# Kernel optimization log

Hardware: AMD Instinct MI355X
Metric: run time of the kernel (lower is better)

## Reference

```python
import jax, jax.numpy as jnp
import numpy as np

HEADS, DIM_HEAD, LANDMARKS, PINV_ITERS, CONV_K = 8, 64, 256, 6, 33


def iter_pinv(x, iters=PINV_ITERS):
    # Moore-Penrose iterative pseudo-inverse (lucidrains nystrom_attention)
    abs_x = jnp.abs(x)
    scale = abs_x.sum(-1).max() * abs_x.sum(-2).max()  # global maxes, as in torch.max
    z = jnp.swapaxes(x, -1, -2) / scale
    I = jnp.eye(x.shape[-1], dtype=x.dtype)
    for _ in range(iters):
        xz = x @ z
        z = 0.25 * z @ (13.0 * I - xz @ (15.0 * I - xz @ (7.0 * I - xz)))
    return z


def nystrom_attention(h, W_qkv, W_out, b_out, conv_w):
    b, n, _ = h.shape
    inner = HEADS * DIM_HEAD
    qkv = h @ W_qkv  # (b, n, 3*inner), bias=False
    q, k, v = jnp.split(qkv, 3, axis=-1)
    split_heads = lambda t: t.reshape(b, n, HEADS, DIM_HEAD).transpose(0, 2, 1, 3)
    q, k, v = split_heads(q), split_heads(k), split_heads(v)  # (b,h,n,dh)
    q = q * (DIM_HEAD ** -0.5)
    l = n // LANDMARKS  # tokens per landmark (n divisible by m, so no padding)
    q_l = q.reshape(b, HEADS, LANDMARKS, l, DIM_HEAD).mean(3)
    k_l = k.reshape(b, HEADS, LANDMARKS, l, DIM_HEAD).mean(3)
    sim1 = jnp.einsum('bhnd,bhmd->bhnm', q, k_l)      # (b,h,n,m)
    sim2 = jnp.einsum('bhmd,bhld->bhml', q_l, k_l)    # (b,h,m,m)
    sim3 = jnp.einsum('bhmd,bhnd->bhmn', q_l, k)      # (b,h,m,n)
    attn1 = jax.nn.softmax(sim1, -1)
    attn2 = jax.nn.softmax(sim2, -1)
    attn3 = jax.nn.softmax(sim3, -1)
    out = (attn1 @ iter_pinv(attn2)) @ (attn3 @ v)    # (b,h,n,dh)
    # residual depthwise conv along sequence dim: Conv2d(heads, heads, (33,1), groups=heads, no bias)
    res = jax.lax.conv_general_dilated(
        v, conv_w, window_strides=(1, 1),
        padding=((CONV_K // 2, CONV_K // 2), (0, 0)),
        feature_group_count=HEADS)
    out = out + res
    out = out.transpose(0, 2, 1, 3).reshape(b, n, inner)
    return out @ W_out + b_out


def setup_inputs() -> dict:
    key = jax.random.key(0)
    ks = jax.random.split(key, 8)
    N, Din, Dout = 8192, 1024, 256
    inner = HEADS * DIM_HEAD
    s = 0.02
    return {
        'x': jax.random.normal(ks[0], (1, N, Din), jnp.float32),
        'W_ft': jax.random.normal(ks[1], (Din, Dout), jnp.float32) * s,
        'b_ft': jnp.zeros((Dout,), jnp.float32),
        'W_qkv': jax.random.normal(ks[2], (Dout, 3 * inner), jnp.float32) * s,
        'W_out': jax.random.normal(ks[3], (inner, Dout), jnp.float32) * s,
        'b_out': jnp.zeros((Dout,), jnp.float32),
        'conv_w': jax.random.normal(ks[4], (HEADS, 1, CONV_K, 1), jnp.float32) * s,
        'W_score': jax.random.normal(ks[5], (Dout, 1), jnp.float32) * s,
        'b_score': jnp.zeros((1,), jnp.float32),
    }


def reference(x, W_ft, b_ft, W_qkv, W_out, b_out, conv_w, W_score, b_score):
    # feature_transform: Linear -> Dropout (identity in eval) -> ReLU
    h = jax.nn.relu(x @ W_ft + b_ft)                 # (1, N, Dout)
    af = nystrom_attention(h, W_qkv, W_out, b_out, conv_w)
    # score_layer: Linear -> Dropout -> ReLU
    scores = jax.nn.relu(af @ W_score + b_score)     # (1, N, 1)
    scores = scores[0].T                             # (1, N)
    weights = jax.nn.softmax(scores, axis=1)         # (1, N)
    aggregated = weights @ h[0]                      # (1, Dout)
    return aggregated, weights
```

## Files before the change

kernel.cpp:

```cpp
#include <hip/hip_runtime.h>

typedef unsigned short u16;
typedef __attribute__((ext_vector_type(8))) short s16x8;
typedef __attribute__((ext_vector_type(4))) float f32x4;
typedef __attribute__((ext_vector_type(8))) unsigned short u16x8;

__device__ inline float b2f(u16 u) {
  unsigned x = ((unsigned)u) << 16;
  return __builtin_bit_cast(float, x);
}
__device__ inline u16 f2b(float f) {
  unsigned u = __builtin_bit_cast(unsigned, f);
  u += 0x7fffu + ((u >> 16) & 1u);
  return (u16)(u >> 16);
}

#define GLL(src, dst) __builtin_amdgcn_global_load_lds( \
    (const __attribute__((address_space(1))) unsigned int*)(src), \
    (__attribute__((address_space(3))) unsigned int*)(dst), 16, 0, 0)

struct MP {
  const u16* A; const u16* B;
  u16* C; u16* Ct; float* Cf; u16* vTo;
  const u16* Aadd; const float* bias;
// ... 167 lines not shown
  const int bz = blockIdx.z, head = bz >> 4, kc = bz & 15;
  const u16* S = p.S + (size_t)head * 256 * 8192 + kc * 512;
  const u16* B = p.vT + (size_t)head * 524288 + kc * 512;
  const int m0 = blockIdx.y * 128;
  const int srow = lane & 15, skoff = (lane >> 4) * 8;
  const int wm0 = (wid >> 1) * 64, wn0 = (wid & 1) * 32;

  int rowA[2]; float am[2], ai[2];
#pragma unroll
  for (int ap = 0; ap < 2; ap++) {
    rowA[ap] = m0 + (wid + ap * 4) * 16 + srow;
    float2 s2 = p.st[head * 256 + rowA[ap]];
    am[ap] = s2.x; ai[ap] = s2.y;
  }

  f32x4 acc[4][2];
#pragma unroll
  for (int i = 0; i < 4; i++)
#pragma unroll
    for (int j = 0; j < 2; j++) acc[i][j] = (f32x4){0.f, 0.f, 0.f, 0.f};

  u16x8 areg[2];
  auto load_a = [&](int kt) {
#pragma unroll
    for (int ap = 0; ap < 2; ap++)
      areg[ap] = *(const u16x8*)(S + (size_t)rowA[ap] * 8192 + kt + skoff);
  };
  auto write_a = [&](int sb) {
#pragma unroll
    for (int ap = 0; ap < 2; ap++) {
      int pp = wid + ap * 4;
      u16 t[8];
#pragma unroll
      for (int e = 0; e < 8; e++)
        t[e] = f2b(expf(b2f(areg[ap][e]) - am[ap]) * ai[ap]);
      *(s16x8*)&lds[sb * (NPAN * 512) + pp * 512 + lane * 8] = *(const s16x8*)t;
    }
  };
  auto stage_b = [&](int sb, int kt) {
    int pp = 8 + wid;
    const u16* src = B + (size_t)((pp - 8) * 16 + srow) * 8192 + kt + skoff;
    GLL(src, &lds[sb * (NPAN * 512) + pp * 512]);
  };
  auto compute = [&](int sb) {
    const int bo = sb * (NPAN * 512);
    s16x8 afr[4], bfr[2];
#pragma unroll
    for (int i = 0; i < 4; i++)
      afr[i] = *(const s16x8*)&lds[bo + (wm0 / 16 + i) * 512 + lane * 8];
#pragma unroll
    for (int j = 0; j < 2; j++)
      bfr[j] = *(const s16x8*)&lds[bo + (APAN + wn0 / 16 + j) * 512 + lane * 8];
#pragma unroll
    for (int i = 0; i < 4; i++)
#pragma unroll
      for (int j = 0; j < 2; j++)
        acc[i][j] = __builtin_amdgcn_mfma_f32_16x16x32_bf16(afr[i], bfr[j], acc[i][j], 0, 0, 0);
  };

  const int nt = 16;
  int buf = 0;
  load_a(0); stage_b(0, 0); write_a(0);
  asm volatile("s_waitcnt vmcnt(0)" ::: "memory");
  __syncthreads();
  for (int t = 0; t < nt; ++t) {
    if (t + 1 < nt) { load_a((t + 1) * 32); stage_b(buf ^ 1, (t + 1) * 32); }
    compute(buf);
    if (t + 1 < nt) write_a(buf ^ 1);
    asm volatile("s_waitcnt vmcnt(0)" ::: "memory");
    __syncthreads();
    buf ^= 1;
  }

  const int r0 = (lane >> 4) * 4, c0 = lane & 15;
#pragma unroll
  for (int i = 0; i < 4; i++)
#pragma unroll
    for (int j = 0; j < 2; j++)
#pragma unroll
      for (int q = 0; q < 4; q++) {
        const int gr = m0 + wm0 + i * 16 + r0 + q;
        const int gc = wn0 + j * 16 + c0;
        p.Cf[(size_t)bz * 16384 + (size_t)gr * 64 + gc] = acc[i][j][q];
      }
}

struct FA1 { const u16 *qkvb, *kl, *MmT; u16 *af; };

__global__ __launch_bounds__(256) void fused_attn1(FA1 p)
{
  __shared__ __align__(16) u16 lds[36864];
  __shared__ float mb[4][64];
  const int tid = threadIdx.x, lane = tid & 63, wid = tid >> 6;
  const int head = blockIdx.y, n0 = blockIdx.x * 64;
  const int srow = lane & 15, skoff = (lane >> 4) * 8;
  const int rbase = (lane >> 4) * 4;

  for (int pid = wid; pid < 72; pid += 4) {
    const u16* src;
    if (pid < 8) {
      int pr = pid >> 1, kc = pid & 1;
      src = p.qkvb + (size_t)(n0 + pr * 16 + srow) * 1536 + head * 64 + kc * 32 + skoff;
    } else if (pid < 40) {
      int j = pid - 8, pr = j >> 1, kc = j & 1;
      src = p.kl + head * 16384 + (size_t)(pr * 16 + srow) * 64 + kc * 32 + skoff;
    } else {
      int j = pid - 40, pr = j >> 3, kc = j & 7;
      src = p.MmT + head * 16384 + (size_t)(pr * 16 + srow) * 256 + kc * 32 + skoff;
    }
    GLL(src, &lds[pid * 512]);
  }
  asm volatile("s_waitcnt vmcnt(0)" ::: "memory");
  __syncthreads();

  const int wr = (wid >> 1) * 32, ch_ = wid & 1;
  f32x4 s[2][8];
#pragma unroll
  for (int i = 0; i < 2; i++)
#pragma unroll
    for (int j = 0; j < 8; j++) s[i][j] = (f32x4){0.f, 0.f, 0.f, 0.f};
#pragma unroll
  for (int t = 0; t < 2; t++) {
    s16x8 a[2], b[8];
#pragma unroll
    for (int i = 0; i < 2; i++)
      a[i] = *(const s16x8*)&lds[(((wid >> 1) * 2 + i) * 2 + t) * 512 + lane * 8];
#pragma unroll
    for (int j = 0; j < 8; j++)
      b[j] = *(const s16x8*)&lds[4096 + ((ch_ * 8 + j) * 2 + t) * 512 + lane * 8];
#pragma unroll
    for (int i = 0; i < 2; i++)
#pragma unroll
      for (int j = 0; j < 8; j++)
        s[i][j] = __builtin_amdgcn_mfma_f32_16x16x32_bf16(a[i], b[j], s[i][j], 0, 0, 0);
  }
#pragma unroll
  for (int i = 0; i < 2; i++)
#pragma unroll
    for (int q = 0; q < 4; q++) {
      float rm = -INFINITY;
#pragma unroll
      for (int j = 0; j < 8; j++) rm = fmaxf(rm, s[i][j][q]);
#pragma unroll
      for (int off = 1; off < 16; off <<= 1) rm = fmaxf(rm, __shfl_xor(rm, off));
      if ((lane & 15) == 0) mb[ch_][wr + i * 16 + rbase + q] = rm;
    }
  __syncthreads();
  float m_[2][4];
#pragma unroll
  for (int i = 0; i < 2; i++)
#pragma unroll
    for (int q = 0; q < 4; q++)
      m_[i][q] = fmaxf(mb[0][wr + i * 16 + rbase + q], mb[1][wr + i * 16 + rbase + q]);
#pragma unroll
  for (int i = 0; i < 2; i++)
#pragma unroll
    for (int q = 0; q < 4; q++) {
      float ss = 0.f;
#pragma unroll
      for (int j = 0; j < 8; j++) {
        float e = expf(s[i][j][q] - m_[i][q]);
        s[i][j][q] = e; ss += e;
      }
#pragma unroll
      for (int off = 1; off < 16; off <<= 1) ss += __shfl_xor(ss, off);
      if ((lane & 15) == 0) mb[2 + ch_][wr + i * 16 + rbase + q] = ss;
    }
  __syncthreads();
#pragma unroll
  for (int i = 0; i < 2; i++)
#pragma unroll
    for (int q = 0; q < 4; q++) {
      int row = wr + i * 16 + rbase + q;
      float inv = 1.f / (mb[2][row] + mb[3][row]);
#pragma unroll
      for (int j = 0; j < 8; j++)
        lds[(size_t)row * 264 + ch_ * 128 + j * 16 + (lane & 15)] = f2b(s[i][j][q] * inv);
    }
  __syncthreads();
  const int wr2 = (wid >> 1) * 32, wd2 = (wid & 1) * 32;
  f32x4 acc[2][2];
#pragma unroll
  for (int i = 0; i < 2; i++)
#pragma unroll
    for (int jd = 0; jd < 2; jd++) acc[i][jd] = (f32x4){0.f, 0.f, 0.f, 0.f};
#pragma unroll
  for (int t = 0; t < 8; t++) {
    s16x8 a[2], b[2];
#pragma unroll
    for (int i = 0; i < 2; i++)
      a[i] = *(const s16x8*)&lds[(size_t)(wr2 + i * 16 + (lane & 15)) * 264 + t * 32 + (lane >> 4) * 8];
#pragma unroll
    for (int jd = 0; jd < 2; jd++)
      b[jd] = *(const s16x8*)&lds[20480 + (((wid & 1) * 2 + jd) * 8 + t) * 512 + lane * 8];
#pragma unroll
    for (int i = 0; i < 2; i++)
#pragma unroll
      for (int jd = 0; jd < 2; jd++)
        acc[i][jd] = __builtin_amdgcn_mfma_f32_16x16x32_bf16(a[i], b[jd], acc[i][jd], 0, 0, 0);
  }
#pragma unroll
  for (int i = 0; i < 2; i++)
#pragma unroll
    for (int jd = 0; jd < 2; jd++)
#pragma unroll
      for (int q = 0; q < 4; q++)
        p.af[(size_t)(n0 + wr2 + i * 16 + rbase + q) * 512 + head * 64 + wd2 + jd * 16 + (lane & 15)]
            = f2b(acc[i][jd][q]);
}

__global__ void conv_res_add_bf16(const u16* __restrict__ qkvb,
                                  const float* __restrict__ convw,
                                  u16* __restrict__ af)
{
  __shared__ float vt[96][64];
  const int h = blockIdx.y, n0 = blockIdx.x * 64;
  const int t = threadIdx.x, ch = t & 63, r0 = t >> 6;
  for (int r = r0; r < 96; r += 4) {
    int n = n0 - 16 + r;
    float v = 0.f;
    if (n >= 0 && n < 8192) v = b2f(qkvb[(size_t)n * 1536 + 1024 + h * 64 + ch]);
    vt[r][ch] = v;
  }
  __syncthreads();
  float w[33];
#pragma unroll
  for (int j = 0; j < 33; j++) w[j] = convw[h * 33 + j];
  for (int tl = r0; tl < 64; tl += 4) {
    float acc = 0.f;
#pragma unroll
    for (int j = 0; j < 33; j++) acc += w[j] * vt[tl + j][ch];
    size_t o = (size_t)(n0 + tl) * 512 + h * 64 + ch;
    af[o] = f2b(b2f(af[o]) + acc);
  }
}

__global__ void reduce_bias_bf16(const float* __restrict__ parts, int nparts,
                                 const float* __restrict__ bias, int relu,
                                 u16* __restrict__ out,
                                 const float* __restrict__ Wscore,
                                 const float* __restrict__ bscore,
                                 float* __restrict__ scores)
{
  const int i4 = blockIdx.x * 256 + threadIdx.x;
  float4 s = ((const float4*)parts)[i4];
  for (int k = 1; k < nparts; k++) {
    float4 v = ((const float4*)parts)[(size_t)k * 524288 + i4];
    s.x += v.x; s.y += v.y; s.z += v.z; s.w += v.w;
  }
  const float4 b = ((const float4*)bias)[i4 & 63];
  s.x += b.x; s.y += b.y; s.z += b.z; s.w += b.w;
  if (relu) {
    s.x = fmaxf(s.x, 0.f); s.y = fmaxf(s.y, 0.f);
    s.z = fmaxf(s.z, 0.f); s.w = fmaxf(s.w, 0.f);
  }
  if (out) {
    ushort4 o; o.x = f2b(s.x); o.y = f2b(s.y); o.z = f2b(s.z); o.w = f2b(s.w);
    ((ushort4*)out)[i4] = o;
  }
  if (Wscore) {
    const int lane = threadIdx.x & 63;
    const float4 w = ((const float4*)Wscore)[lane];
    float v = s.x * w.x + s.y * w.y + s.z * w.z + s.w * w.w;
    for (int off = 32; off; off >>= 1) v += __shfl_down(v, off);
    if (lane == 0)
      scores[blockIdx.x * 4 + (threadIdx.x >> 6)] = fmaxf(v + bscore[0], 0.f);
  }
}

__global__ void fused_tail(const float* __restrict__ scores,
                           const u16* __restrict__ hb, float* __restrict__ out)
{
  __shared__ float red[256];
  const int t = threadIdx.x, c = blockIdx.x;
  float e[32];
  float m = -INFINITY;
#pragma unroll
  for (int i = 0; i < 32; i++) { e[i] = scores[t + i * 256]; m = fmaxf(m, e[i]); }
  red[t] = m; __syncthreads();
  for (int s = 128; s; s >>= 1) { if (t < s) red[t] = fmaxf(red[t], red[t + s]); __syncthreads(); }
  m = red[0]; __syncthreads();
  float ls = 0.f;
#pragma unroll
  for (int i = 0; i < 32; i++) { e[i] = expf(e[i] - m); ls += e[i]; }
  red[t] = ls; __syncthreads();
  for (int s = 128; s; s >>= 1) { if (t < s) red[t] += red[t + s]; __syncthreads(); }
  const float inv = 1.f / red[0];
  __syncthreads();

  if (c < 256) {
    float acc = 0.f;
#pragma unroll
    for (int i = 0; i < 32; i++)
      acc += e[i] * inv * b2f(hb[(size_t)(t + i * 256) * 256 + c]);
    red[t] = acc; __syncthreads();
    for (int s = 128; s; s >>= 1) { if (t < s) red[t] += red[t + s]; __syncthreads(); }
    if (t == 0) out[c] = red[0];
  } else {
#pragma unroll
    for (int i = 0; i < 32; i++) out[256 + t + i * 256] = e[i] * inv;
  }
}

__global__ void prescale(const u16* __restrict__ x2, float* __restrict__ sbuf)
{
  const int h = blockIdx.x, t = threadIdx.x;
  const u16* X = x2 + ((size_t)h << 16);
  float cs = 0.f;
  for (int r = 0; r < 256; r++) cs += fabsf(b2f(X[r * 256 + t]));
  float rs = 0.f;
  for (int c4 = 0; c4 < 256; c4 += 4) {
    ushort4 v = *(const ushort4*)(X + (size_t)t * 256 + c4);
    rs += fabsf(b2f(v.x)) + fabsf(b2f(v.y)) + fabsf(b2f(v.z)) + fabsf(b2f(v.w));
  }
  __shared__ float red[512];
  red[t] = rs; red[256 + t] = cs;
  __syncthreads();
  for (int s = 128; s; s >>= 1) {
    if (t < s) {
      red[t] = fmaxf(red[t], red[t + s]);
      red[256 + t] = fmaxf(red[256 + t], red[256 + t + s]);
    }
    __syncthreads();
  }
  if (t == 0) { sbuf[h] = red[0]; sbuf[8 + h] = red[256]; }
}

__global__ void pinv_init(const u16* __restrict__ x2, const float* __restrict__ sbuf,
                          u16* __restrict__ z0, u16* __restrict__ z0T)
{
  __shared__ u16 tile[64][80];
  const int t = threadIdx.x;
  const size_t base = (size_t)blockIdx.y << 16;
  const int tr = (blockIdx.x >> 2) * 64, tc = (blockIdx.x & 3) * 64;
  const u16* X = x2 + base;

  float mr = -INFINITY, mc = -INFINITY;
#pragma unroll
  for (int i = 0; i < 8; i++) {
    mr = fmaxf(mr, sbuf[i]);
    mc = fmaxf(mc, sbuf[8 + i]);
  }
  const float inv = 1.f / (mr * mc);

  {
    int r = t >> 2, cg = (t & 3) * 16;
#pragma unroll
    for (int v4 = 0; v4 < 4; v4++) {
      ushort4 v = *(const ushort4*)(X + (size_t)(tr + r) * 256 + tc + cg + v4 * 4);
      v.x = f2b(b2f(v.x) * inv); v.y = f2b(b2f(v.y) * inv);
      v.z = f2b(b2f(v.z) * inv); v.w = f2b(b2f(v.w) * inv);
      *(ushort4*)(z0T + base + (size_t)(tr + r) * 256 + tc + cg + v4 * 4) = v;
      *(ushort4*)&tile[r][cg + v4 * 4] = v;
    }
  }
  __syncthreads();
  {
    int c = t >> 2, rg = (t & 3) * 16;
    u16 o[16];
#pragma unroll
    for (int e = 0; e < 16; e++) o[e] = tile[rg + e][c];
#pragma unroll
    for (int v4 = 0; v4 < 4; v4++)
      *(ushort4*)(z0 + base + (size_t)(tc + c) * 256 + tr + rg + v4 * 4) = *(ushort4*)&o[v4 * 4];
  }
}

struct PG {
  const u16 *U, *V, *Xadd, *XaddT;
  u16 *DR, *DT;
  float alpha, beta;
};

template<bool WD, bool WDT>
__global__ __launch_bounds__(256) void pinv_gemm(PG p)
{
  __shared__ __align__(16) u16 lds[65536 / 2];
  const int tid = threadIdx.x, lane = tid & 63, wid = tid >> 6;
  const size_t base = (size_t)blockIdx.z << 16;
  const u16* U = p.U + base;
  const u16* V = p.V + base;
  const int m0 = blockIdx.y * 64, n0 = blockIdx.x * 64;
  const int srow = lane & 15, skoff = (lane >> 4) * 8;
  const int wr = (wid >> 1) * 32, wc = (wid & 1) * 32;

#pragma unroll
  for (int q = 0; q < 16; q++) {
    const int pid = wid * 16 + q;
    const int rg = (pid >> 3) & 3, t = pid & 7;
    const u16* src = (pid < 32)
      ? U + (size_t)(m0 + rg * 16 + srow) * 256 + t * 32 + skoff
      : V + (size_t)(n0 + rg * 16 + srow) * 256 + t * 32 + skoff;
    GLL(src, &lds[pid * 512]);
  }
  asm volatile("s_waitcnt vmcnt(0)" ::: "memory");
  __syncthreads();

  f32x4 acc[2][2], accT[2][2];
#pragma unroll
  for (int i = 0; i < 2; i++)
#pragma unroll
    for (int j = 0; j < 2; j++) {
      acc[i][j] = (f32x4){0.f, 0.f, 0.f, 0.f};
      accT[i][j] = (f32x4){0.f, 0.f, 0.f, 0.f};
    }

#pragma unroll
  for (int t = 0; t < 8; t++) {
    s16x8 afr[2], bfr[2];
#pragma unroll
    for (int i = 0; i < 2; i++)
      afr[i] = *(const s16x8*)&lds[((wr / 16 + i) * 8 + t) * 512 + lane * 8];
#pragma unroll
    for (int j = 0; j < 2; j++)
      bfr[j] = *(const s16x8*)&lds[(32 + (wc / 16 + j) * 8 + t) * 512 + lane * 8];
#pragma unroll
    for (int i = 0; i < 2; i++)
#pragma unroll
      for (int j = 0; j < 2; j++) {
        if constexpr (WD)
          acc[i][j] = __builtin_amdgcn_mfma_f32_16x16x32_bf16(afr[i], bfr[j], acc[i][j], 0, 0, 0);
        if constexpr (WDT)
          accT[j][i] = __builtin_amdgcn_mfma_f32_16x16x32_bf16(bfr[j], afr[i], accT[j][i], 0, 0, 0);
      }
  }

  const int r0 = (lane >> 4) * 4, c0 = lane & 15;
  if constexpr (WD) {
    const u16* Xa = p.Xadd ? p.Xadd + base : nullptr;
    u16* DR = p.DR + base;
#pragma unroll
    for (int i = 0; i < 2; i++)
#pragma unroll
      for (int j = 0; j < 2; j++)
#pragma unroll
        for (int q = 0; q < 4; q++) {
          const int gr = m0 + wr + i * 16 + r0 + q;
          const int gc = n0 + wc + j * 16 + c0;
          float v = p.alpha * acc[i][j][q];
          if (Xa) v += p.beta * b2f(Xa[(size_t)gr * 256 + gc]);
          DR[(size_t)gr * 256 + gc] = f2b(v);
        }
  }
  if constexpr (WDT) {
    const u16* Xt = p.XaddT ? p.XaddT + base : nullptr;
    u16* DT = p.DT + base;
#pragma unroll
    for (int j = 0; j < 2; j++)
#pragma unroll
      for (int i = 0; i < 2; i++)
#pragma unroll
        for (int q = 0; q < 4; q++) {
          const int gn = n0 + wc + j * 16 + r0 + q;
          const int gm = m0 + wr + i * 16 + c0;
          float v = p.alpha * accT[j][i][q];
          if (Xt) v += p.beta * b2f(Xt[(size_t)gn * 256 + gm]);
          DT[(size_t)gn * 256 + gm] = f2b(v);
        }
  }
}

struct PR1 { const u16 *A, *At, *z; u16 *B, *Bt, *G, *Gt, *W; };

__global__ __launch_bounds__(256) void pinv_r1(PR1 p)
{
  __shared__ __align__(16) u16 lds[32768];
  const int tid = threadIdx.x, lane = tid & 63, wid = tid >> 6;
  const int prob = blockIdx.z >> 3;
  const size_t base = (size_t)(blockIdx.z & 7) << 16;
  const u16* U = (prob ? p.z : p.A) + base;
  const u16* V = p.At + base;
  const int m0 = blockIdx.y * 64, n0 = blockIdx.x * 64;
  const int srow = lane & 15, skoff = (lane >> 4) * 8;
  const int wr = (wid >> 1) * 32, wc = (wid & 1) * 32;

#pragma unroll
  for (int q = 0; q < 16; q++) {
    const int pid = wid * 16 + q;
    const int rg = (pid >> 3) & 3, t = pid & 7;
    const u16* src = (pid < 32)
      ? U + (size_t)(m0 + rg * 16 + srow) * 256 + t * 32 + skoff
      : V + (size_t)(n0 + rg * 16 + srow) * 256 + t * 32 + skoff;
    GLL(src, &lds[pid * 512]);
  }
  asm volatile("s_waitcnt vmcnt(0)" ::: "memory");
  __syncthreads();

  f32x4 acc[2][2], accT[2][2];
#pragma unroll
  for (int i = 0; i < 2; i++)
#pragma unroll
    for (int j = 0; j < 2; j++) {
      acc[i][j] = (f32x4){0.f, 0.f, 0.f, 0.f};
      accT[i][j] = (f32x4){0.f, 0.f, 0.f, 0.f};
    }

#pragma unroll
  for (int t = 0; t < 8; t++) {
    s16x8 afr[2], bfr[2];
#pragma unroll
    for (int i = 0; i < 2; i++)
      afr[i] = *(const s16x8*)&lds[((wr / 16 + i) * 8 + t) * 512 + lane * 8];
#pragma unroll
    for (int j = 0; j < 2; j++)
      bfr[j] = *(const s16x8*)&lds[(32 + (wc / 16 + j) * 8 + t) * 512 + lane * 8];
#pragma unroll
    for (int i = 0; i < 2; i++)
#pragma unroll
      for (int j = 0; j < 2; j++) {
        acc[i][j] = __builtin_amdgcn_mfma_f32_16x16x32_bf16(afr[i], bfr[j], acc[i][j], 0, 0, 0);
        if (prob == 0)
          accT[j][i] = __builtin_amdgcn_mfma_f32_16x16x32_bf16(bfr[j], afr[i], accT[j][i], 0, 0, 0);
      }
  }

  const int r0 = (lane >> 4) * 4, c0 = lane & 15;
  if (prob == 0) {
    const u16* Ab  = p.A  + base;
    const u16* Atb = p.At + base;
    u16 *Bv = p.B + base, *Btv = p.Bt + base;
    u16 *Gv = p.G + base, *Gtv = p.Gt + base;
#pragma unroll
    for (int i = 0; i < 2; i++)
#pragma unroll
      for (int j = 0; j < 2; j++)
#pragma unroll
        for (int q = 0; q < 4; q++) {
          const int gr = m0 + wr + i * 16 + r0 + q;
          const int gc = n0 + wc + j * 16 + c0;
          float b = acc[i][j][q];
          float a = b2f(Ab[(size_t)gr * 256 + gc]);
          Bv[(size_t)gr * 256 + gc] = f2b(b);
          Gv[(size_t)gr * 256 + gc] = f2b(7.f * a - b);
        }
#pragma unroll
    for (int j = 0; j < 2; j++)
#pragma unroll
      for (int i = 0; i < 2; i++)
#pragma unroll
        for (int q = 0; q < 4; q++) {
          const int gn = n0 + wc + j * 16 + r0 + q;
          const int gm = m0 + wr + i * 16 + c0;
          float bt = accT[j][i][q];
          float at = b2f(Atb[(size_t)gn * 256 + gm]);
          Btv[(size_t)gn * 256 + gm] = f2b(bt);
          Gtv[(size_t)gn * 256 + gm] = f2b(7.f * at - bt);
        }
  } else {
    u16* Wv = p.W + base;
#pragma unroll
    for (int i = 0; i < 2; i++)
#pragma unroll
      for (int j = 0; j < 2; j++)
#pragma unroll
        for (int q = 0; q < 4; q++) {
          const int gr = m0 + wr + i * 16 + r0 + q;
          const int gc = n0 + wc + j * 16 + c0;
          Wv[(size_t)gr * 256 + gc] = f2b(acc[i][j][q]);
        }
  }
}

struct PR2 { const u16 *W, *G, *Gt, *B, *Bt, *z, *A, *At; u16 *zo, *Ao, *Aot; };

__global__ __launch_bounds__(256) void pinv_r2(PR2 p)
{
  __shared__ __align__(16) u16 lds[32768];
  const int tid = threadIdx.x, lane = tid & 63, wid = tid >> 6;
  const int prob = blockIdx.z >> 3;
  const size_t base = (size_t)(blockIdx.z & 7) << 16;
  const u16* U = (prob ? p.G  : p.W ) + base;
  const u16* V = (prob ? p.Bt : p.Gt) + base;
  const int m0 = blockIdx.y * 64, n0 = blockIdx.x * 64;
  const int srow = lane & 15, skoff = (lane >> 4) * 8;
  const int wr = (wid >> 1) * 32, wc = (wid & 1) * 32;

#pragma unroll
  for (int q = 0; q < 16; q++) {
    const int pid = wid * 16 + q;
    const int rg = (pid >> 3) & 3, t = pid & 7;
    const u16* src = (pid < 32)
      ? U + (size_t)(m0 + rg * 16 + srow) * 256 + t * 32 + skoff
      : V + (size_t)(n0 + rg * 16 + srow) * 256 + t * 32 + skoff;
    GLL(src, &lds[pid * 512]);
  }
  asm volatile("s_waitcnt vmcnt(0)" ::: "memory");
  __syncthreads();

  f32x4 acc[2][2], accT[2][2];
#pragma unroll
  for (int i = 0; i < 2; i++)
#pragma unroll
    for (int j = 0; j < 2; j++) {
      acc[i][j] = (f32x4){0.f, 0.f, 0.f, 0.f};
      accT[i][j] = (f32x4){0.f, 0.f, 0.f, 0.f};
    }

#pragma unroll
  for (int t = 0; t < 8; t++) {
    s16x8 afr[2], bfr[2];
#pragma unroll
    for (int i = 0; i < 2; i++)
      afr[i] = *(const s16x8*)&lds[((wr / 16 + i) * 8 + t) * 512 + lane * 8];
#pragma unroll
    for (int j = 0; j < 2; j++)
      bfr[j] = *(const s16x8*)&lds[(32 + (wc / 16 + j) * 8 + t) * 512 + lane * 8];
#pragma unroll
    for (int i = 0; i < 2; i++)
#pragma unroll
      for (int j = 0; j < 2; j++) {
        acc[i][j] = __builtin_amdgcn_mfma_f32_16x16x32_bf16(afr[i], bfr[j], acc[i][j], 0, 0, 0);
        if (prob)
          accT[j][i] = __builtin_amdgcn_mfma_f32_16x16x32_bf16(bfr[j], afr[i], accT[j][i], 0, 0, 0);
      }
  }

  const int r0 = (lane >> 4) * 4, c0 = lane & 15;
  if (prob == 0) {
    const u16* Zb = p.z + base;
    const u16* Wb = p.W + base;
    u16* Zo = p.zo + base;
#pragma unroll
    for (int i = 0; i < 2; i++)
#pragma unroll
      for (int j = 0; j < 2; j++)
#pragma unroll
        for (int q = 0; q < 4; q++) {
          const int gr = m0 + wr + i * 16 + r0 + q;
          const int gc = n0 + wc + j * 16 + c0;
          float v = 0.25f * acc[i][j][q]
                  + 3.25f * b2f(Zb[(size_t)gr * 256 + gc])
                  - 3.75f * b2f(Wb[(size_t)gr * 256 + gc]);
          Zo[(size_t)gr * 256 + gc] = f2b(v);
        }
  } else {
    const u16* Ab  = p.A  + base;
    const u16* Bb  = p.B  + base;
    const u16* Atb = p.At + base;
    const u16* Btb = p.Bt + base;
    u16* Ao  = p.Ao  + base;
    u16* Aot = p.Aot + base;
#pragma unroll
    for (int i = 0; i < 2; i++)
#pragma unroll
      for (int j = 0; j < 2; j++)
#pragma unroll
        for (int q = 0; q < 4; q++) {
          const int gr = m0 + wr + i * 16 + r0 + q;
          const int gc = n0 + wc + j * 16 + c0;
          float v = 0.25f * acc[i][j][q]
                  + 3.25f * b2f(Ab[(size_t)gr * 256 + gc])
                  - 3.75f * b2f(Bb[(size_t)gr * 256 + gc]);
          Ao[(size_t)gr * 256 + gc] = f2b(v);
        }
#pragma unroll
    for (int j = 0; j < 2; j++)
#pragma unroll
      for (int i = 0; i < 2; i++)
#pragma unroll
        for (int q = 0; q < 4; q++) {
          const int gn = n0 + wc + j * 16 + r0 + q;
          const int gm = m0 + wr + i * 16 + c0;
          float v = 0.25f * accT[j][i][q]
                  + 3.25f * b2f(Atb[(size_t)gn * 256 + gm])
                  - 3.75f * b2f(Btb[(size_t)gn * 256 + gm]);
          Aot[(size_t)gn * 256 + gm] = f2b(v);
        }
  }
}

__global__ void prep_weights(const float* __restrict__ Wft, const float* __restrict__ Wqkv,
                             const float* __restrict__ Wout, u16* __restrict__ WftT,
                             u16* __restrict__ WqkvT, u16* __restrict__ WoutT)
{
  int idx = blockIdx.x * 256 + threadIdx.x;
  if (idx < 262144) {
    int r = idx & 1023, c = idx >> 10;
    WftT[idx] = f2b(Wft[(size_t)r * 256 + c]);
  } else if (idx < 655360) {
    int i = idx - 262144;
    int r = i & 255, c = i >> 8;
    WqkvT[i] = f2b(Wqkv[(size_t)r * 1536 + c]);
  } else {
    int i = idx - 655360;
    int r = i & 511, c = i >> 9;
    WoutT[i] = f2b(Wout[(size_t)r * 256 + c]);
  }
}

__global__ void landmark_means(const u16* __restrict__ qkvb,
                               u16* __restrict__ ql, u16* __restrict__ kl)
{
  int idx = blockIdx.x * 256 + threadIdx.x;
  int which = idx >> 17, r = idx & 131071;
  int h = r >> 14, m = (r >> 6) & 255, d = r & 63;
  const u16* src = qkvb + (which ? 512 : 0) + h * 64 + d;
  float s = 0.f; int n0 = m * 32;
  for (int i = 0; i < 32; i++) s += b2f(src[(size_t)(n0 + i) * 1536]);
  (which ? kl : ql)[r] = f2b(s * (1.f / 32.f));
}

__global__ void softmax_rows_bf16_256(u16* __restrict__ d)
{
  const int row = blockIdx.x * 4 + (threadIdx.x >> 6);
  const int lane = threadIdx.x & 63;
  ushort4* p = (ushort4*)(d + (size_t)row * 256);
  ushort4 raw = p[lane];
  float v0 = b2f(raw.x), v1 = b2f(raw.y), v2 = b2f(raw.z), v3 = b2f(raw.w);
  float mx = fmaxf(fmaxf(v0, v1), fmaxf(v2, v3));
  for (int off = 1; off < 64; off <<= 1) mx = fmaxf(mx, __shfl_xor(mx, off));
  v0 = expf(v0 - mx); v1 = expf(v1 - mx); v2 = expf(v2 - mx); v3 = expf(v3 - mx);
  float s = v0 + v1 + v2 + v3;
  for (int off = 1; off < 64; off <<= 1) s += __shfl_xor(s, off);
  float inv = 1.f / s;
  raw.x = f2b(v0 * inv); raw.y = f2b(v1 * inv); raw.z = f2b(v2 * inv); raw.w = f2b(v3 * inv);
  p[lane] = raw;
}

__global__ void reduce_avT(const float* __restrict__ avp, u16* __restrict__ avT)
{
  int idx = blockIdx.x * 256 + threadIdx.x;
  int m = idx & 255, d = (idx >> 8) & 63, h = idx >> 14;
  float s = 0.f;
  for (int c = 0; c < 16; c++) s += avp[((size_t)(h * 16 + c)) * 16384 + m * 64 + d];
  avT[((size_t)h * 64 + d) * 256 + m] = f2b(s);
}

extern "C" void kernel_launch(void* const* d_in, const int* in_sizes, int n_in,
                              void* d_out, int out_size, void* d_ws, size_t ws_size,
                              hipStream_t stream)
{
  const float* x       = (const float*)d_in[0];
  const float* W_ft    = (const float*)d_in[1];
  const float* b_ft    = (const float*)d_in[2];
  const float* W_qkv   = (const float*)d_in[3];
  const float* W_out   = (const float*)d_in[4];
  const float* b_out   = (const float*)d_in[5];
  const float* conv_w  = (const float*)d_in[6];
  const float* W_score = (const float*)d_in[7];
  const float* b_score = (const float*)d_in[8];
  float* out = (float*)d_out;

  char* W = (char*)d_ws;
  auto alloc = [&](size_t bytes) { char* r = W; W += (bytes + 255) & ~(size_t)255; return r; };
  u16* WftT  = (u16*)alloc(256ull * 1024 * 2);
  u16* WqkvT = (u16*)alloc(1536ull * 256 * 2);
  u16* WoutT = (u16*)alloc(256ull * 512 * 2);
  u16* hb    = (u16*)alloc(8192ull * 256 * 2);
  u16* qkvb  = (u16*)alloc(8192ull * 1536 * 2);
  u16* ql    = (u16*)alloc(8ull * 256 * 64 * 2);
  u16* kl    = (u16*)alloc(8ull * 256 * 64 * 2);
  u16* x2    = (u16*)alloc(8ull * 256 * 256 * 2);
  u16* z0    = (u16*)alloc(8ull * 256 * 256 * 2);
  u16* z0T   = (u16*)alloc(8ull * 256 * 256 * 2);
  u16* zp    = (u16*)alloc(8ull * 256 * 256 * 2);
  u16* Amat  = (u16*)alloc(8ull * 256 * 256 * 2);
  u16* AmatT = (u16*)alloc(8ull * 256 * 256 * 2);
  u16* Am2   = (u16*)alloc(8ull * 256 * 256 * 2);
  u16* Am2T  = (u16*)alloc(8ull * 256 * 256 * 2);
  u16* Bm    = (u16*)alloc(8ull * 256 * 256 * 2);
  u16* BmT   = (u16*)alloc(8ull * 256 * 256 * 2);
  u16* Gm    = (u16*)alloc(8ull * 256 * 256 * 2);
  u16* GmT   = (u16*)alloc(8ull * 256 * 256 * 2);
  u16* Wm    = (u16*)alloc(8ull * 256 * 256 * 2);
  u16* BUF   = (u16*)alloc(8ull * 8192 * 256 * 2);
  u16* vT    = (u16*)alloc(8ull * 64 * 8192 * 2);
  float* avp = (float*)alloc(8ull * 16 * 256 * 64 * 4);
  u16* avT   = (u16*)alloc(8ull * 64 * 256 * 2);
  u16* MmT   = (u16*)alloc(8ull * 64 * 256 * 2);
  u16* af    = (u16*)alloc(8192ull * 512 * 2);
  float* gpart = (float*)alloc(4ull * 8192 * 256 * 4);
  float2* stat = (float2*)alloc(2048 * 8);
  float* sbuf   = (float*)alloc(256);
  float* scores = (float*)alloc(8192 * 4);

  auto mp = [](const u16* A, const u16* B, int M, int N, int K,
               int lda, int ldb, long long bA, long long bB) {
    MP p{}; p.A = A; p.B = B; p.M = M; p.N = N; p.K = K;
    p.lda = lda; p.ldb = ldb; p.bA = bA; p.bB = bB;
    p.alpha = 1.f; p.beta = 0.f; p.kchunks = 1; return p;
  };

  prep_weights<<<3072, 256, 0, stream>>>(W_ft, W_qkv, W_out, WftT, WqkvT, WoutT);

  { MP p = mp((const u16*)x, WftT, 8192, 256, 256, 1024, 1024, 0, 0);
    p.kchunks = 4; p.Cf = gpart; p.ldcf = 256; p.bCf = 2097152;
    gemm_mfma<64, 256, true><<<dim3(1, 128, 4), 256, 0, stream>>>(p); }
  reduce_bias_bf16<<<2048, 256, 0, stream>>>(gpart, 4, b_ft, 1, hb,
                                             nullptr, nullptr, nullptr);

  { MP p = mp(hb, WqkvT, 8192, 1536, 256, 256, 256, 0, 0);
    p.C = qkvb; p.ldc = 1536; p.scale_cols = 512; p.colscale = 0.125f; p.vTo = vT;
    gemm_mfma<128, 128, false><<<dim3(12, 64, 1), 256, 0, stream>>>(p); }

  landmark_means<<<1024, 256, 0, stream>>>(qkvb, ql, kl);

  { MP p = mp(ql, kl, 256, 256, 64, 64, 64, 16384, 16384);
    p.C = x2; p.ldc = 256; p.bC = 65536;
    gemm_mfma<64, 64, false><<<dim3(4, 4, 8), 256, 0, stream>>>(p); }
  softmax_rows_bf16_256<<<512, 256, 0, stream>>>(x2);

  prescale<<<8, 256, 0, stream>>>(x2, sbuf);
  pinv_init<<<dim3(16, 8), 256, 0, stream>>>(x2, sbuf, z0, z0T);
  { PG p{x2, z0T, nullptr, nullptr, Amat, AmatT, 1.f, 0.f};
    pinv_gemm<true, true><<<dim3(4, 4, 8), 256, 0, stream>>>(p); }
  {
    const dim3 b(256);
    u16 *zr = z0, *zo = zp;
    u16 *Ar = Amat, *Art = AmatT, *Ao = Am2, *Aot = Am2T;
    for (int it = 0; it < 6; it++) {
      { PR1 r{Ar, Art, zr, Bm, BmT, Gm, GmT, Wm};
        pinv_r1<<<dim3(4, 4, 16), b, 0, stream>>>(r); }
      { PR2 r{Wm, Gm, GmT, Bm, BmT, zr, Ar, Art, zo, Ao, Aot};
        pinv_r2<<<dim3(4, 4, (it == 5) ? 8 : 16), b, 0, stream>>>(r); }
      u16* t;
      t = zr; zr = zo; zo = t;
      t = Ar; Ar = Ao; Ao = t;
      t = Art; Art = Aot; Aot = t;
    }
  }

  { MP p = mp(ql, qkvb + 512, 256, 8192, 64, 64, 1536, 16384, 64);
    p.C = BUF; p.ldc = 8192; p.bC = (long long)256 * 8192;
    gemm_mfma<128, 128, false><<<dim3(64, 2, 8), 256, 0, stream>>>(p); }
  row_stats_8192<<<2048, 256, 0, stream>>>(BUF, stat);

  { AVP p{BUF, stat, vT, avp};
    av_gemm_exp<<<dim3(1, 2, 128), 256, 0, stream>>>(p); }
  reduce_avT<<<512, 256, 0, stream>>>(avp, avT);

  { MP p = mp(z0, avT, 256, 64, 256, 256, 256, 65536, 16384);
    p.Ct = MmT; p.ldct = 256; p.bCt = 16384;
    gemm_mfma<64, 64, false><<<dim3(1, 4, 8), 256, 0, stream>>>(p); }

  { FA1 fp{qkvb, kl, MmT, af};
    fused_attn1<<<dim3(128, 8), 256, 0, stream>>>(fp); }

  conv_res_add_bf16<<<dim3(128, 8), 256, 0, stream>>>(qkvb, conv_w, af);

  { MP p = mp(af, WoutT, 8192, 256, 128, 512, 512, 0, 0);
    p.kchunks = 4; p.Cf = gpart; p.ldcf = 256; p.bCf = 2097152;
    gemm_mfma<64, 256, false><<<dim3(1, 128, 4), 256, 0, stream>>>(p); }
  reduce_bias_bf16<<<2048, 256, 0, stream>>>(gpart, 4, b_out, 0, nullptr,
                                             W_score, b_score, scores);

  fused_tail<<<257, 256, 0, stream>>>(scores, hb, out);
}
```

Measured before the change: 379.1 us.

## Fuse pinv prescale, init and iterations into one persistent kernel with grid barriers

Replaces the 15 separate launches for the iterative pseudo-inverse (prescale, init, first gemm, and six pairs of r1/r2 gemms) with a single persistent kernel of 256 blocks. Stages are separated by a software grid barrier built on an atomic counter, which prep_weights resets to zero at the start. This is meant to remove per-launch overhead and the tail gaps between small dependent kernels. The trade-off is that correctness depends on all 256 blocks being resident at once, and every stage now pays an atomic-spin barrier across the whole grid.

```diff
diff --git a/kernel.cpp b/kernel.cpp
--- a/kernel.cpp
+++ b/kernel.cpp
@@ -493,9 +493,30 @@
   }
 }
 
-__global__ void prescale(const u16* __restrict__ x2, float* __restrict__ sbuf)
-{
-  const int h = blockIdx.x, t = threadIdx.x;
+struct PP {
+  const u16* x2; float* sbuf;
+  u16 *z0, *z0T, *zp;
+  u16 *Am, *AmT, *Am2, *Am2T;
+  u16 *B, *Bt, *G, *Gt, *W;
+  unsigned* cnt;
+};
+
+__device__ __forceinline__ void gbar(unsigned* cnt, unsigned target)
+{
+  __syncthreads();
+  if (threadIdx.x == 0) {
+    __threadfence();
+    __hip_atomic_fetch_add(cnt, 1u, __ATOMIC_RELAXED, __HIP_MEMORY_SCOPE_AGENT);
+    while (__hip_atomic_load(cnt, __ATOMIC_RELAXED, __HIP_MEMORY_SCOPE_AGENT) < target)
+      __builtin_amdgcn_s_sleep(2);
+    __threadfence();
+  }
+  __syncthreads();
+}
+
+__device__ __forceinline__ void prescale_body(const u16* x2, float* sbuf,
+                                              int h, int t, float* red)
+{
   const u16* X = x2 + ((size_t)h << 16);
   float cs = 0.f;
   for (int r = 0; r < 256; r++) cs += fabsf(b2f(X[r * 256 + t]));
@@ -504,7 +525,6 @@
     ushort4 v = *(const ushort4*)(X + (size_t)t * 256 + c4);
     rs += fabsf(b2f(v.x)) + fabsf(b2f(v.y)) + fabsf(b2f(v.z)) + fabsf(b2f(v.w));
   }
-  __shared__ float red[512];
   red[t] = rs; red[256 + t] = cs;
   __syncthreads();
   for (int s = 128; s; s >>= 1) {
@@ -517,13 +537,13 @@
   if (t == 0) { sbuf[h] = red[0]; sbuf[8 + h] = red[256]; }
 }
 
-__global__ void pinv_init(const u16* __restrict__ x2, const float* __restrict__ sbuf,
-                          u16* __restrict__ z0, u16* __restrict__ z0T)
-{
-  __shared__ u16 tile[64][80];
-  const int t = threadIdx.x;
-  const size_t base = (size_t)blockIdx.y << 16;
-  const int tr = (blockIdx.x >> 2) * 64, tc = (blockIdx.x & 3) * 64;
+__device__ __forceinline__ void init_body(const u16* x2, const float* sbuf,
+                                          u16* z0, u16* z0T, int tileIdx, int head,
+                                          int t, u16* smem)
+{
+  u16 (*tile)[80] = reinterpret_cast<u16(*)[80]>(smem);
+  const size_t base = (size_t)head << 16;
+  const int tr = (tileIdx >> 2) * 64, tc = (tileIdx & 3) * 64;
   const u16* X = x2 + base;
 
   float mr = -INFINITY, mc = -INFINITY;
@@ -557,37 +577,24 @@
   }
 }
 
-struct PG {
-  const u16 *U, *V, *Xadd, *XaddT;
-  u16 *DR, *DT;
-  float alpha, beta;
-};
-
-template<bool WD, bool WDT>
-__global__ __launch_bounds__(256) void pinv_gemm(PG p)
-{
-  __shared__ __align__(16) u16 lds[65536 / 2];
-  const int tid = threadIdx.x, lane = tid & 63, wid = tid >> 6;
-  const size_t base = (size_t)blockIdx.z << 16;
-  const u16* U = p.U + base;
-  const u16* V = p.V + base;
-  const int m0 = blockIdx.y * 64, n0 = blockIdx.x * 64;
+__device__ __forceinline__ void pgemm(const u16* U, const u16* V, u16* lds,
+                                      int m0, int n0, int lane, int wid, bool doT,
+                                      f32x4 (&acc)[2][2], f32x4 (&accT)[2][2])
+{
   const int srow = lane & 15, skoff = (lane >> 4) * 8;
-  const int wr = (wid >> 1) * 32, wc = (wid & 1) * 32;
-
 #pragma unroll
   for (int q = 0; q < 16; q++) {
     const int pid = wid * 16 + q;
-    const int rg = (pid >> 3) & 3, t = pid & 7;
+    const int rg = (pid >> 3) & 3, tt = pid & 7;
     const u16* src = (pid < 32)
-      ? U + (size_t)(m0 + rg * 16 + srow) * 256 + t * 32 + skoff
-      : V + (size_t)(n0 + rg * 16 + srow) * 256 + t * 32 + skoff;
+      ? U + (size_t)(m0 + rg * 16 + srow) * 256 + tt * 32 + skoff
+      : V + (size_t)(n0 + rg * 16 + srow) * 256 + tt * 32 + skoff;
     GLL(src, &lds[pid * 512]);
   }
   asm volatile("s_waitcnt vmcnt(0)" ::: "memory");
   __syncthreads();
 
-  f32x4 acc[2][2], accT[2][2];
+  const int wr = (wid >> 1) * 32, wc = (wid & 1) * 32;
 #pragma unroll
   for (int i = 0; i < 2; i++)
 #pragma unroll
@@ -595,7 +602,6 @@
       acc[i][j] = (f32x4){0.f, 0.f, 0.f, 0.f};
       accT[i][j] = (f32x4){0.f, 0.f, 0.f, 0.f};
     }
-
 #pragma unroll
   for (int t = 0; t < 8; t++) {
     s16x8 afr[2], bfr[2];
@@ -609,17 +615,37 @@
     for (int i = 0; i < 2; i++)
 #pragma unroll
       for (int j = 0; j < 2; j++) {
-        if constexpr (WD)
-          acc[i][j] = __builtin_amdgcn_mfma_f32_16x16x32_bf16(afr[i], bfr[j], acc[i][j], 0, 0, 0);
-        if constexpr (WDT)
+        acc[i][j] = __builtin_amdgcn_mfma_f32_16x16x32_bf16(afr[i], bfr[j], acc[i][j], 0, 0, 0);
+        if (doT)
           accT[j][i] = __builtin_amdgcn_mfma_f32_16x16x32_bf16(bfr[j], afr[i], accT[j][i], 0, 0, 0);
       }
   }
-
+}
+
+__global__ __launch_bounds__(256) void pinv_persist(PP p)
+{
+  __shared__ __align__(16) u16 smem[16384];
+  const int bid = blockIdx.x, tid = threadIdx.x;
+  const int lane = tid & 63, wid = tid >> 6;
+  unsigned* cnt = p.cnt;
+
+  if (bid < 8) prescale_body(p.x2, p.sbuf, bid, tid, (float*)smem);
+  gbar(cnt, 256u);
+
+  if (bid < 128) init_body(p.x2, p.sbuf, p.z0, p.z0T, bid & 15, bid >> 4, tid, smem);
+  gbar(cnt, 512u);
+
+  const int bx = bid & 3, by = (bid >> 2) & 3, bz = bid >> 4;
+  const int m0 = by * 64, n0 = bx * 64;
+  const int wr = (wid >> 1) * 32, wc = (wid & 1) * 32;
   const int r0 = (lane >> 4) * 4, c0 = lane & 15;
-  if constexpr (WD) {
-    const u16* Xa = p.Xadd ? p.Xadd + base : nullptr;
-    u16* DR = p.DR + base;
+
+  if (bid < 128) {
+    const size_t base = (size_t)bz << 16;
+    f32x4 acc[2][2], accT[2][2];
+    pgemm(p.x2 + base, p.z0T + base, smem, m0, n0, lane, wid, true, acc, accT);
+    u16* DR = p.Am + base;
+    u16* DT = p.AmT + base;
 #pragma unroll
     for (int i = 0; i < 2; i++)
 #pragma unroll
@@ -628,14 +654,8 @@
         for (int q = 0; q < 4; q++) {
           const int gr = m0 + wr + i * 16 + r0 + q;
           const int gc = n0 + wc + j * 16 + c0;
-          float v = p.alpha * acc[i][j][q];
-          if (Xa) v += p.beta * b2f(Xa[(size_t)gr * 256 + gc]);
-          DR[(size_t)gr * 256 + gc] = f2b(v);
+          DR[(size_t)gr * 256 + gc] = f2b(acc[i][j][q]);
         }
-  }
-  if constexpr (WDT) {
-    const u16* Xt = p.XaddT ? p.XaddT + base : nullptr;
-    u16* DT = p.DT + base;
 #pragma unroll
     for (int j = 0; j < 2; j++)
 #pragma unroll
@@ -644,227 +664,141 @@
         for (int q = 0; q < 4; q++) {
           const int gn = n0 + wc + j * 16 + r0 + q;
           const int gm = m0 + wr + i * 16 + c0;
-          float v = p.alpha * accT[j][i][q];
-          if (Xt) v += p.beta * b2f(Xt[(size_t)gn * 256 + gm]);
-          DT[(size_t)gn * 256 + gm] = f2b(v);
+          DT[(size_t)gn * 256 + gm] = f2b(accT[j][i][q]);
         }
   }
-}
-
-struct PR1 { const u16 *A, *At, *z; u16 *B, *Bt, *G, *Gt, *W; };
-
-__global__ __launch_bounds__(256) void pinv_r1(PR1 p)
-{
-  __shared__ __align__(16) u16 lds[32768];
-  const int tid = threadIdx.x, lane = tid & 63, wid = tid >> 6;
-  const int prob = blockIdx.z >> 3;
-  const size_t base = (size_t)(blockIdx.z & 7) << 16;
-  const u16* U = (prob ? p.z : p.A) + base;
-  const u16* V = p.At + base;
-  const int m0 = blockIdx.y * 64, n0 = blockIdx.x * 64;
-  const int srow = lane & 15, skoff = (lane >> 4) * 8;
-  const int wr = (wid >> 1) * 32, wc = (wid & 1) * 32;
-
-#pragma unroll
-  for (int q = 0; q < 16; q++) {
-    const int pid = wid * 16 + q;
-    const int rg = (pid >> 3) & 3, t = pid & 7;
-    const u16* src = (pid < 32)
-      ? U + (size_t)(m0 + rg * 16 + srow) * 256 + t * 32 + skoff
-      : V + (size_t)(n0 + rg * 16 + srow) * 256 + t * 32 + skoff;
-    GLL(src, &lds[pid * 512]);
-  }
-  asm volatile("s_waitcnt vmcnt(0)" ::: "memory");
-  __syncthreads();
-
-  f32x4 acc[2][2], accT[2][2];
-#pragma unroll
-  for (int i = 0; i < 2; i++)
-#pragma unroll
-    for (int j = 0; j < 2; j++) {
-      acc[i][j] = (f32x4){0.f, 0.f, 0.f, 0.f};
-      accT[i][j] = (f32x4){0.f, 0.f, 0.f, 0.f};
-    }
-
-#pragma unroll
-  for (int t = 0; t < 8; t++) {
-    s16x8 afr[2], bfr[2];
-#pragma unroll
-    for (int i = 0; i < 2; i++)
-      afr[i] = *(const s16x8*)&lds[((wr / 16 + i) * 8 + t) * 512 + lane * 8];
-#pragma unroll
-    for (int j = 0; j < 2; j++)
-      bfr[j] = *(const s16x8*)&lds[(32 + (wc / 16 + j) * 8 + t) * 512 + lane * 8];
-#pragma unroll
-    for (int i = 0; i < 2; i++)
-#pragma unroll
-      for (int j = 0; j < 2; j++) {
-        acc[i][j] = __builtin_amdgcn_mfma_f32_16x16x32_bf16(afr[i], bfr[j], acc[i][j], 0, 0, 0);
-        if (prob == 0)
-          accT[j][i] = __builtin_amdgcn_mfma_f32_16x16x32_bf16(bfr[j], afr[i], accT[j][i], 0, 0, 0);
+  unsigned tgt = 768u;
+  gbar(cnt, tgt);
+
+  u16 *zr = p.z0, *zo = p.zp;
+  u16 *Ar = p.Am, *Art = p.AmT, *Ao = p.Am2, *Aot = p.Am2T;
+  const int prob = bz >> 3;
+  const size_t base = (size_t)(bz & 7) << 16;
+
+  for (int it = 0; it < 6; it++) {
+    {
+      f32x4 acc[2][2], accT[2][2];
+      pgemm((prob ? zr : Ar) + base, Art + base, smem, m0, n0, lane, wid,
+            prob == 0, acc, accT);
+      if (prob == 0) {
+        const u16* Ab  = Ar  + base;
+        const u16* Atb = Art + base;
+        u16 *Bv = p.B + base, *Btv = p.Bt + base;
+        u16 *Gv = p.G + base, *Gtv = p.Gt + base;
+#pragma unroll
+        for (int i = 0; i < 2; i++)
+#pragma unroll
+          for (int j = 0; j < 2; j++)
+#pragma unroll
+            for (int q = 0; q < 4; q++) {
+              const int gr = m0 + wr + i * 16 + r0 + q;
+              const int gc = n0 + wc + j * 16 + c0;
+              float b = acc[i][j][q];
+              float a = b2f(Ab[(size_t)gr * 256 + gc]);
+              Bv[(size_t)gr * 256 + gc] = f2b(b);
+              Gv[(size_t)gr * 256 + gc] = f2b(7.f * a - b);
+            }
+#pragma unroll
+        for (int j = 0; j < 2; j++)
+#pragma unroll
+          for (int i = 0; i < 2; i++)
+#pragma unroll
+            for (int q = 0; q < 4; q++) {
+              const int gn = n0 + wc + j * 16 + r0 + q;
+              const int gm = m0 + wr + i * 16 + c0;
+              float bt = accT[j][i][q];
+              float at = b2f(Atb[(size_t)gn * 256 + gm]);
+              Btv[(size_t)gn * 256 + gm] = f2b(bt);
+              Gtv[(size_t)gn * 256 + gm] = f2b(7.f * at - bt);
+            }
+      } else {
+        u16* Wv = p.W + base;
+#pragma unroll
+        for (int i = 0; i < 2; i++)
+#pragma unroll
+          for (int j = 0; j < 2; j++)
+#pragma unroll
+            for (int q = 0; q < 4; q++) {
+              const int gr = m0 + wr + i * 16 + r0 + q;
+              const int gc = n0 + wc + j * 16 + c0;
+              Wv[(size_t)gr * 256 + gc] = f2b(acc[i][j][q]);
+            }
       }
-  }
-
-  const int r0 = (lane >> 4) * 4, c0 = lane & 15;
-  if (prob == 0) {
-    const u16* Ab  = p.A  + base;
-    const u16* Atb = p.At + base;
-    u16 *Bv = p.B + base, *Btv = p.Bt + base;
-    u16 *Gv = p.G + base, *Gtv = p.Gt + base;
-#pragma unroll
-    for (int i = 0; i < 2; i++)
-#pragma unroll
-      for (int j = 0; j < 2; j++)
-#pragma unroll
-        for (int q = 0; q < 4; q++) {
-          const int gr = m0 + wr + i * 16 + r0 + q;
-          const int gc = n0 + wc + j * 16 + c0;
-          float b = acc[i][j][q];
-          float a = b2f(Ab[(size_t)gr * 256 + gc]);
-          Bv[(size_t)gr * 256 + gc] = f2b(b);
-          Gv[(size_t)gr * 256 + gc] = f2b(7.f * a - b);
-        }
-#pragma unroll
-    for (int j = 0; j < 2; j++)
-#pragma unroll
-      for (int i = 0; i < 2; i++)
-#pragma unroll
-        for (int q = 0; q < 4; q++) {
-          const int gn = n0 + wc + j * 16 + r0 + q;
-          const int gm = m0 + wr + i * 16 + c0;
-          float bt = accT[j][i][q];
-          float at = b2f(Atb[(size_t)gn * 256 + gm]);
-          Btv[(size_t)gn * 256 + gm] = f2b(bt);
-          Gtv[(size_t)gn * 256 + gm] = f2b(7.f * at - bt);
-        }
-  } else {
-    u16* Wv = p.W + base;
-#pragma unroll
-    for (int i = 0; i < 2; i++)
-#pragma unroll
-      for (int j = 0; j < 2; j++)
-#pragma unroll
-        for (int q = 0; q < 4; q++) {
-          const int gr = m0 + wr + i * 16 + r0 + q;
-          const int gc = n0 + wc + j * 16 + c0;
-          Wv[(size_t)gr * 256 + gc] = f2b(acc[i][j][q]);
-        }
-  }
-}
-
-struct PR2 { const u16 *W, *G, *Gt, *B, *Bt, *z, *A, *At; u16 *zo, *Ao, *Aot; };
-
-__global__ __launch_bounds__(256) void pinv_r2(PR2 p)
-{
-  __shared__ __align__(16) u16 lds[32768];
-  const int tid = threadIdx.x, lane = tid & 63, wid = tid >> 6;
-  const int prob = blockIdx.z >> 3;
-  const size_t base = (size_t)(blockIdx.z & 7) << 16;
-  const u16* U = (prob ? p.G  : p.W ) + base;
-  const u16* V = (prob ? p.Bt : p.Gt) + base;
-  const int m0 = blockIdx.y * 64, n0 = blockIdx.x * 64;
-  const int srow = lane & 15, skoff = (lane >> 4) * 8;
-  const int wr = (wid >> 1) * 32, wc = (wid & 1) * 32;
-
-#pragma unroll
-  for (int q = 0; q < 16; q++) {
-    const int pid = wid * 16 + q;
-    const int rg = (pid >> 3) & 3, t = pid & 7;
-    const u16* src = (pid < 32)
-      ? U + (size_t)(m0 + rg * 16 + srow) * 256 + t * 32 + skoff
-      : V + (size_t)(n0 + rg * 16 + srow) * 256 + t * 32 + skoff;
-    GLL(src, &lds[pid * 512]);
-  }
-  asm volatile("s_waitcnt vmcnt(0)" ::: "memory");
-  __syncthreads();
-
-  f32x4 acc[2][2], accT[2][2];
-#pragma unroll
-  for (int i = 0; i < 2; i++)
-#pragma unroll
-    for (int j = 0; j < 2; j++) {
-      acc[i][j] = (f32x4){0.f, 0.f, 0.f, 0.f};
-      accT[i][j] = (f32x4){0.f, 0.f, 0.f, 0.f};
-    }
-
-#pragma unroll
-  for (int t = 0; t < 8; t++) {
-    s16x8 afr[2], bfr[2];
-#pragma unroll
-    for (int i = 0; i < 2; i++)
-      afr[i] = *(const s16x8*)&lds[((wr / 16 + i) * 8 + t) * 512 + lane * 8];
-#pragma unroll
-    for (int j = 0; j < 2; j++)
-      bfr[j] = *(const s16x8*)&lds[(32 + (wc / 16 + j) * 8 + t) * 512 + lane * 8];
-#pragma unroll
-    for (int i = 0; i < 2; i++)
-#pragma unroll
-      for (int j = 0; j < 2; j++) {
-        acc[i][j] = __builtin_amdgcn_mfma_f32_16x16x32_bf16(afr[i], bfr[j], acc[i][j], 0, 0, 0);
-        if (prob)
-          accT[j][i] = __builtin_amdgcn_mfma_f32_16x16x32_bf16(bfr[j], afr[i], accT[j][i], 0, 0, 0);
+    }
+    tgt += 256u; gbar(cnt, tgt);
+
+    if (!(it == 5 && prob == 1)) {
+      f32x4 acc[2][2], accT[2][2];
+      pgemm((prob ? p.G : p.W) + base, (prob ? p.Bt : p.Gt) + base, smem,
+            m0, n0, lane, wid, prob == 1, acc, accT);
+      if (prob == 0) {
+        const u16* Zb = zr + base;
+        const u16* Wb = p.W + base;
+        u16* Zo = zo + base;
+#pragma unroll
+        for (int i = 0; i < 2; i++)
+#pragma unroll
+          for (int j = 0; j < 2; j++)
+#pragma unroll
+            for (int q = 0; q < 4; q++) {
+              const int gr = m0 + wr + i * 16 + r0 + q;
+              const int gc = n0 + wc + j * 16 + c0;
+              float v = 0.25f * acc[i][j][q]
+                      + 3.25f * b2f(Zb[(size_t)gr * 256 + gc])
+                      - 3.75f * b2f(Wb[(size_t)gr * 256 + gc]);
+              Zo[(size_t)gr * 256 + gc] = f2b(v);
+            }
+      } else {
+        const u16* Ab  = Ar  + base;
+        const u16* Bb  = p.B + base;
+        const u16* Atb = Art + base;
+        const u16* Btb = p.Bt + base;
+        u16* AoP  = Ao  + base;
+        u16* AotP = Aot + base;
+#pragma unroll
+        for (int i = 0; i < 2; i++)
+#pragma unroll
+          for (int j = 0; j < 2; j++)
+#pragma unroll
+            for (int q = 0; q < 4; q++) {
+              const int gr = m0 + wr + i * 16 + r0 + q;
+              const int gc = n0 + wc + j * 16 + c0;
+              float v = 0.25f * acc[i][j][q]
+                      + 3.25f * b2f(Ab[(size_t)gr * 256 + gc])
+                      - 3.75f * b2f(Bb[(size_t)gr * 256 + gc]);
+              AoP[(size_t)gr * 256 + gc] = f2b(v);
+            }
+#pragma unroll
+        for (int j = 0; j < 2; j++)
+#pragma unroll
+          for (int i = 0; i < 2; i++)
+#pragma unroll
+            for (int q = 0; q < 4; q++) {
+              const int gn = n0 + wc + j * 16 + r0 + q;
+              const int gm = m0 + wr + i * 16 + c0;
+              float v = 0.25f * accT[j][i][q]
+                      + 3.25f * b2f(Atb[(size_t)gn * 256 + gm])
+                      - 3.75f * b2f(Btb[(size_t)gn * 256 + gm]);
+              AotP[(size_t)gn * 256 + gm] = f2b(v);
+            }
       }
-  }
-
-  const int r0 = (lane >> 4) * 4, c0 = lane & 15;
-  if (prob == 0) {
-    const u16* Zb = p.z + base;
-    const u16* Wb = p.W + base;
-    u16* Zo = p.zo + base;
-#pragma unroll
-    for (int i = 0; i < 2; i++)
-#pragma unroll
-      for (int j = 0; j < 2; j++)
-#pragma unroll
-        for (int q = 0; q < 4; q++) {
-          const int gr = m0 + wr + i * 16 + r0 + q;
-          const int gc = n0 + wc + j * 16 + c0;
-          float v = 0.25f * acc[i][j][q]
-                  + 3.25f * b2f(Zb[(size_t)gr * 256 + gc])
-                  - 3.75f * b2f(Wb[(size_t)gr * 256 + gc]);
-          Zo[(size_t)gr * 256 + gc] = f2b(v);
-        }
-  } else {
-    const u16* Ab  = p.A  + base;
-    const u16* Bb  = p.B  + base;
-    const u16* Atb = p.At + base;
-    const u16* Btb = p.Bt + base;
-    u16* Ao  = p.Ao  + base;
-    u16* Aot = p.Aot + base;
-#pragma unroll
-    for (int i = 0; i < 2; i++)
-#pragma unroll
-      for (int j = 0; j < 2; j++)
-#pragma unroll
-        for (int q = 0; q < 4; q++) {
-          const int gr = m0 + wr + i * 16 + r0 + q;
-          const int gc = n0 + wc + j * 16 + c0;
-          float v = 0.25f * acc[i][j][q]
-                  + 3.25f * b2f(Ab[(size_t)gr * 256 + gc])
-                  - 3.75f * b2f(Bb[(size_t)gr * 256 + gc]);
-          Ao[(size_t)gr * 256 + gc] = f2b(v);
-        }
-#pragma unroll
-    for (int j = 0; j < 2; j++)
-#pragma unroll
-      for (int i = 0; i < 2; i++)
-#pragma unroll
-        for (int q = 0; q < 4; q++) {
-          const int gn = n0 + wc + j * 16 + r0 + q;
-          const int gm = m0 + wr + i * 16 + c0;
-          float v = 0.25f * accT[j][i][q]
-                  + 3.25f * b2f(Atb[(size_t)gn * 256 + gm])
-                  - 3.75f * b2f(Btb[(size_t)gn * 256 + gm]);
-          Aot[(size_t)gn * 256 + gm] = f2b(v);
-        }
+    }
+    if (it < 5) { tgt += 256u; gbar(cnt, tgt); }
+
+    u16* tp;
+    tp = zr; zr = zo; zo = tp;
+    tp = Ar; Ar = Ao; Ao = tp;
+    tp = Art; Art = Aot; Aot = tp;
   }
 }
 
 __global__ void prep_weights(const float* __restrict__ Wft, const float* __restrict__ Wqkv,
                              const float* __restrict__ Wout, u16* __restrict__ WftT,
-                             u16* __restrict__ WqkvT, u16* __restrict__ WoutT)
+                             u16* __restrict__ WqkvT, u16* __restrict__ WoutT,
+                             unsigned* __restrict__ cnt)
 {
   int idx = blockIdx.x * 256 + threadIdx.x;
+  if (idx == 0) *cnt = 0;
   if (idx < 262144) {
     int r = idx & 1023, c = idx >> 10;
     WftT[idx] = f2b(Wft[(size_t)r * 256 + c]);
@@ -964,6 +898,7 @@
   float2* stat = (float2*)alloc(2048 * 8);
   float* sbuf   = (float*)alloc(256);
   float* scores = (float*)alloc(8192 * 4);
+  unsigned* cntr = (unsigned*)alloc(256);
 
   auto mp = [](const u16* A, const u16* B, int M, int N, int K,
                int lda, int ldb, long long bA, long long bB) {
@@ -972,7 +907,7 @@
     p.alpha = 1.f; p.beta = 0.f; p.kchunks = 1; return p;
   };
 
-  prep_weights<<<3072, 256, 0, stream>>>(W_ft, W_qkv, W_out, WftT, WqkvT, WoutT);
+  prep_weights<<<3072, 256, 0, stream>>>(W_ft, W_qkv, W_out, WftT, WqkvT, WoutT, cntr);
 
   { MP p = mp((const u16*)x, WftT, 8192, 256, 256, 1024, 1024, 0, 0);
     p.kchunks = 4; p.Cf = gpart; p.ldcf = 256; p.bCf = 2097152;
@@ -991,25 +926,8 @@
     gemm_mfma<64, 64, false><<<dim3(4, 4, 8), 256, 0, stream>>>(p); }
   softmax_rows_bf16_256<<<512, 256, 0, stream>>>(x2);
 
-  prescale<<<8, 256, 0, stream>>>(x2, sbuf);
-  pinv_init<<<dim3(16, 8), 256, 0, stream>>>(x2, sbuf, z0, z0T);
-  { PG p{x2, z0T, nullptr, nullptr, Amat, AmatT, 1.f, 0.f};
-    pinv_gemm<true, true><<<dim3(4, 4, 8), 256, 0, stream>>>(p); }
-  {
-    const dim3 b(256);
-    u16 *zr = z0, *zo = zp;
-    u16 *Ar = Amat, *Art = AmatT, *Ao = Am2, *Aot = Am2T;
-    for (int it = 0; it < 6; it++) {
-      { PR1 r{Ar, Art, zr, Bm, BmT, Gm, GmT, Wm};
-        pinv_r1<<<dim3(4, 4, 16), b, 0, stream>>>(r); }
-      { PR2 r{Wm, Gm, GmT, Bm, BmT, zr, Ar, Art, zo, Ao, Aot};
-        pinv_r2<<<dim3(4, 4, (it == 5) ? 8 : 16), b, 0, stream>>>(r); }
-      u16* t;
-      t = zr; zr = zo; zo = t;
-      t = Ar; Ar = Ao; Ao = t;
-      t = Art; Art = Aot; Aot = t;
-    }
-  }
+  { PP pp{x2, sbuf, z0, z0T, zp, Amat, AmatT, Am2, Am2T, Bm, BmT, Gm, GmT, Wm, cntr};
+    pinv_persist<<<256, 256, 0, stream>>>(pp); }
 
   { MP p = mp(ql, qkvb + 512, 256, 8192, 64, 64, 1536, 16384, 64);
     p.C = BUF; p.ldc = 8192; p.bC = (long long)256 * 8192;
```

Measured after the change: 674.9 us. +78.0%, slower.
